# Kernel optimization log

Hardware: AMD Instinct MI355X
Metric: run time of the kernel (lower is better)

The kernel has to match this reference:

```python
import jax, jax.numpy as jnp
import numpy as np

N = 100_000      # nodes
E = 1_600_000    # edges (avg degree 16)
D_IN = 256
D_OUT = 128


def setup_inputs() -> dict:
    key = jax.random.key(0)
    ks = jax.random.split(key, 13)
    stdv = 1.0 / np.sqrt(D_OUT)      # matches reset_parameters
    std_att = 1.0                    # att_vec_* have fan 1 -> stdv 1
    std_av = 1.0 / np.sqrt(3.0)
    return {
        "x": jax.random.normal(ks[0], (N, D_IN), dtype=jnp.float32),
        "edge_src": jax.random.randint(ks[1], (E,), 0, N),
        "edge_dst": jax.random.randint(ks[2], (E,), 0, N),
        "w_low": jax.random.uniform(ks[3], (E,), dtype=jnp.float32) / 16.0,   # ~normalized adj
        "w_high": jax.random.normal(ks[4], (E,), dtype=jnp.float32) / 16.0,    # high-pass weights can be +/-
        "w_unnorm": jax.random.uniform(ks[5], (E,), dtype=jnp.float32),
        "W_low": jax.random.uniform(ks[6], (D_IN, D_OUT), jnp.float32, -stdv, stdv),
        "W_high": jax.random.uniform(ks[7], (D_IN, D_OUT), jnp.float32, -stdv, stdv),
        "W_mlp": jax.random.uniform(ks[8], (D_IN, D_OUT), jnp.float32, -stdv, stdv),
        "a_low": jax.random.uniform(ks[9], (D_OUT, 1), jnp.float32, -std_att, std_att),
        "a_high": jax.random.uniform(ks[10], (D_OUT, 1), jnp.float32, -std_att, std_att),
        "a_mlp": jax.random.uniform(ks[11], (D_OUT, 1), jnp.float32, -std_att, std_att),
        "att_vec": jax.random.uniform(ks[12], (3, 3), jnp.float32, -std_av, std_av),
    }


def _spmm(w, src, dst, h, n):
    # sparse [n,n] @ dense [n,d]: gather source rows, weight, scatter-add to dest
    return jax.ops.segment_sum(w[:, None] * h[src], dst, num_segments=n)


def reference(x, edge_src, edge_dst, w_low, w_high, w_unnorm,
              W_low, W_high, W_mlp, a_low, a_high, a_mlp, att_vec):
    n = x.shape[0]
    # variant=False path: relu(spmm(adj, x @ W))
    h_low = jax.nn.relu(_spmm(w_low, edge_src, edge_dst, x @ W_low, n))
    h_high = jax.nn.relu(_spmm(w_high, edge_src, edge_dst, x @ W_high, n))
    h_mlp = jax.nn.relu(x @ W_mlp)
    # attention3: sigmoid of per-branch scalar scores -> 3x3 mix -> softmax (T=3)
    scores = jnp.concatenate([h_low @ a_low, h_high @ a_high, h_mlp @ a_mlp], axis=1)  # [n,3]
    att = jax.nn.softmax((jax.nn.sigmoid(scores) @ att_vec) / 3.0, axis=1)
    return 3.0 * (att[:, 0:1] * h_low + att[:, 1:2] * h_high + att[:, 2:3] * h_mlp)
```

## Files before the change

### kernel.cpp

```cpp
#include <hip/hip_runtime.h>
#include <hip/hip_bf16.h>
#include <math.h>

#define D_IN   256
#define D_OUT  128
#define NHB    256

typedef __attribute__((ext_vector_type(8))) short short8;
typedef __attribute__((ext_vector_type(4))) float floatx4;

__device__ __forceinline__ unsigned short f2bf(float f) {
  union { float f; unsigned u; } v; v.f = f;
  unsigned r = v.u + 0x7fffu + ((v.u >> 16) & 1u);
  return (unsigned short)(r >> 16);
}

__global__ __launch_bounds__(512) void hist_prep_kernel(
    const float* __restrict__ Wl, const float* __restrict__ Wh,
    const float* __restrict__ Wm, unsigned short* __restrict__ Bpack,
    const int* __restrict__ dst, int* __restrict__ bh, int E, int NB1,
    int* __restrict__ ticket) {
  __shared__ int hist[1024];
  const int bid = blockIdx.x;
  const int t = threadIdx.x;
  if (bid == 0 && t == 0) *ticket = 0;
  if (bid < NHB) {
    for (int k = t; k < NB1; k += 512) hist[k] = 0;
    __syncthreads();
    const int chunk = (E + NHB - 1) / NHB;
    const int base = bid * chunk;
    const int lim = min(E, base + chunk);
    for (int e = base + t; e < lim; e += 512) atomicAdd(&hist[dst[e] >> 7], 1);
    __syncthreads();
    for (int k = t; k < NB1; k += 512) bh[k * NHB + bid] = hist[k];
  } else {
    int tt = (bid - NHB) * 512 + t;
    int j = tt & 7;
    int lane = (tt >> 3) & 63;
    int f = tt >> 9;
    int nt = f % 24, kt = f / 24;
    int k = kt * 32 + (lane >> 4) * 8 + j;
    int n_ = nt * 16 + (lane & 15);
    const float* W = (n_ < 128) ? Wl : (n_ < 256 ? Wh : Wm);
    Bpack[tt] = f2bf(W[k * D_OUT + (n_ & 127)]);
  }
}

__global__ __launch_bounds__(512) void scan_kernel(
    const int* __restrict__ bh, int* __restrict__ bhscan,
    int* __restrict__ bsum, int M, int nscan, int* __restrict__ ticket) {
  __shared__ int sd[512];
  __shared__ int lastFlag;
  const int sb = blockIdx.x;
  const int t = threadIdx.x;
  int base = sb * 2048 + t * 4;
  int v0 = base + 0 < M ? bh[base + 0] : 0;
  int v1 = base + 1 < M ? bh[base + 1] : 0;
  int v2 = base + 2 < M ? bh[base + 2] : 0;
  int v3 = base + 3 < M ? bh[base + 3] : 0;
  int tsum = v0 + v1 + v2 + v3;
  sd[t] = tsum;
  __syncthreads();
  for (int off = 1; off < 512; off <<= 1) {
    int add = (t >= off) ? sd[t - off] : 0;
    __syncthreads();
    sd[t] += add;
    __syncthreads();
  }
  int excl = sd[t] - tsum;
  if (base + 0 < M) bhscan[base + 0] = excl;
  if (base + 1 < M) bhscan[base + 1] = excl + v0;
  if (base + 2 < M) bhscan[base + 2] = excl + v0 + v1;
  if (base + 3 < M) bhscan[base + 3] = excl + v0 + v1 + v2;
  if (t == 511) {
    bsum[sb] = sd[511];
    __threadfence();
    int prev = atomicAdd(ticket, 1);
    lastFlag = (prev == nscan - 1);
  }
  __syncthreads();
  if (!lastFlag) return;
  __threadfence();
  int v = t < nscan ? bsum[t] : 0;
  sd[t] = v;
  __syncthreads();
  for (int off = 1; off < 512; off <<= 1) {
    int add = (t >= off) ? sd[t - off] : 0;
    __syncthreads();
    sd[t] += add;
    __syncthreads();
  }
  if (t < nscan) bsum[t] = sd[t] - v;
}

#define LDSROW 392
__global__ __launch_bounds__(512, 4) void gemm_sort_kernel(
    const float* __restrict__ x,
    const unsigned short* __restrict__ Bpack, unsigned short* __restrict__ Zg,
    unsigned short* __restrict__ Zm, int n_nodes, const int* __restrict__ src,
    const int* __restrict__ dst, const float* __restrict__ wlo,
    const float* __restrict__ whi, const int* __restrict__ bhscan,
    const int* __restrict__ bsum, uint2* __restrict__ tmp, int E, int NB1) {
  __shared__ unsigned short lds[16384];
  const int bid = blockIdx.x;

  int gemm_id;
  if (bid < 2 * NHB) {
    if ((bid & 1) == 0) {
      int rb = bid >> 1;
      int* cur = (int*)lds;
      int t = threadIdx.x;
      for (int k = t; k < NB1; k += 512) {
        int idx = k * NHB + rb;
        cur[k] = bhscan[idx] + bsum[idx >> 11];
      }
      __syncthreads();
      const int chunk = (E + NHB - 1) / NHB;
      const int base = rb * chunk;
      const int lim = min(E, base + chunk);
      for (int e = base + t; e < lim; e += 512) {
        int d = dst[e];
        int pos = atomicAdd(&cur[d >> 7], 1);
        unsigned wl = f2bf(wlo[e]), wh = f2bf(whi[e]);
        tmp[pos] = make_uint2((unsigned)src[e] | ((unsigned)(d & 127) << 20),
                              wl | (wh << 16));
      }
      return;
    }
    gemm_id = bid >> 1;
  } else {
    gemm_id = bid - 2 * NHB + NHB;
  }

  const int lane = threadIdx.x & 63;
  const int w = threadIdx.x >> 6;
  const int rowbase = gemm_id * 64;
  const int m16 = lane & 15, quad = lane >> 4;

  {
    const float4* xf = (const float4*)x;
#pragma unroll
    for (int i = 0; i < 4; i++) {
      int idx = i * 512 + threadIdx.x;
      int row = idx >> 5, c = idx & 31;
      int gr = rowbase + row;
      if (gr > n_nodes - 1) gr = n_nodes - 1;
      float4 f0 = xf[(size_t)gr * 64 + c * 2];
      float4 f1 = xf[(size_t)gr * 64 + c * 2 + 1];
      unsigned w0, w1, w2, w3;
      asm("v_cvt_pk_bf16_f32 %0, %1, %2" : "=v"(w0) : "v"(f0.x), "v"(f0.y));
      asm("v_cvt_pk_bf16_f32 %0, %1, %2" : "=v"(w1) : "v"(f0.z), "v"(f0.w));
      asm("v_cvt_pk_bf16_f32 %0, %1, %2" : "=v"(w2) : "v"(f1.x), "v"(f1.y));
      asm("v_cvt_pk_bf16_f32 %0, %1, %2" : "=v"(w3) : "v"(f1.z), "v"(f1.w));
      union { uint4 u; short8 s8; } cv;
      cv.u = make_uint4(w0, w1, w2, w3);
      int pc = (c & ~7) | ((c ^ row) & 7);
      ((short8*)lds)[row * 32 + pc] = cv.s8;
    }
  }
  __syncthreads();

  floatx4 acc[4][3];
#pragma unroll
  for (int s = 0; s < 4; s++)
#pragma unroll
    for (int c = 0; c < 3; c++) acc[s][c] = (floatx4)(0.f);

  const short8* bp = (const short8*)Bpack + lane;

#pragma unroll
  for (int kt = 0; kt < 8; kt++) {
    short8 a[4];
#pragma unroll
    for (int s = 0; s < 4; s++) {
      int r_ = s * 16 + m16;
      int c_ = kt * 4 + quad;
      int pc = (c_ & ~7) | ((c_ ^ r_) & 7);
      a[s] = ((const short8*)lds)[r_ * 32 + pc];
    }
#pragma unroll
    for (int c = 0; c < 3; c++) {
      short8 b = bp[(kt * 24 + w * 3 + c) * 64];
#pragma unroll
      for (int s = 0; s < 4; s++)
        acc[s][c] =
            __builtin_amdgcn_mfma_f32_16x16x32_bf16(a[s], b, acc[s][c], 0, 0, 0);
    }
  }

  __syncthreads();
  unsigned short* tile = lds;

#pragma unroll
  for (int half = 0; half < 2; half++) {
    if (half) __syncthreads();
#pragma unroll
    for (int s = 0; s < 2; s++)
#pragma unroll
      for (int c = 0; c < 3; c++)
#pragma unroll
        for (int r = 0; r < 4; r++)
          tile[(s * 16 + quad * 4 + r) * LDSROW + (w * 3 + c) * 16 + m16] =
              f2bf(acc[half * 2 + s][c][r]);
    __syncthreads();
#pragma unroll
    for (int it = 0; it < 3; it++) {
      int chunk = it * 512 + threadIdx.x;
      int row = chunk / 48, c8 = chunk % 48;
      int grow = rowbase + half * 32 + row;
      if (grow < n_nodes) {
        short8 v = *(const short8*)&tile[row * LDSROW + c8 * 8];
        if (c8 < 32)
          *(short8*)(Zg + (size_t)grow * 256 + c8 * 8) = v;
        else
          *(short8*)(Zm + (size_t)grow * 128 + (c8 - 32) * 8) = v;
      }
    }
  }
}

__global__ __launch_bounds__(512) void fine_kernel(
    const uint2* __restrict__ tmp, const int* __restrict__ bhscan,
    const int* __restrict__ bsum, uint2* __restrict__ meta,
    int* __restrict__ rowptr, int NB1, int n, int E) {
  __shared__ int fh[128];
  __shared__ int sd[128];
  __shared__ int cur[128];
  const int b = blockIdx.x;
  const int t = threadIdx.x;
  auto scanidx = [&](int i) { return bhscan[i] + bsum[i >> 11]; };
  const int s0 = scanidx(b * NHB);
  const int s1 = (b == NB1 - 1) ? E : scanidx((b + 1) * NHB);

  if (t < 128) fh[t] = 0;
  __syncthreads();
  for (int i = s0 + t; i < s1; i += 512)
    atomicAdd(&fh[(tmp[i].x >> 20) & 127], 1);
  __syncthreads();

  if (t < 128) sd[t] = fh[t];
  __syncthreads();
  for (int off = 1; off < 128; off <<= 1) {
    int add = (t >= off && t < 128) ? sd[t - off] : 0;
    __syncthreads();
    if (t < 128) sd[t] += add;
    __syncthreads();
  }
  if (t < 128) {
    int excl = sd[t] - fh[t];
    cur[t] = excl;
    int node = b * 128 + t;
    if (node < n) rowptr[node] = s0 + excl;
  }
  if (b == 0 && t == 0) rowptr[n] = E;
  __syncthreads();

  for (int i = s0 + t; i < s1; i += 512) {
    uint2 v = tmp[i];
    int d = (v.x >> 20) & 127;
    int pos = s0 + atomicAdd(&cur[d], 1);
    meta[pos] = make_uint2(v.x & 0xFFFFFu, v.y);
  }
}

__global__ __launch_bounds__(128) void node_kernel(
    const unsigned short* __restrict__ Zg, const unsigned short* __restrict__ Zm,
    const int* __restrict__ rowptr, const unsigned long long* __restrict__ meta,
    const float* __restrict__ a_low, const float* __restrict__ a_high,
    const float* __restrict__ a_mlp, const float* __restrict__ att_vec,
    float* __restrict__ out, int n_nodes) {
  int node = blockIdx.x * 2 + (threadIdx.x >> 6);
  if (node >= n_nodes) return;
  node = __builtin_amdgcn_readfirstlane(node);
  const int lane = threadIdx.x & 63;
  const int isHigh = lane >> 5;
  const int dbase = (lane & 31) * 4;
  const char* Zb = (const char*)Zg;

  const int start = rowptr[node];
  const int end = rowptr[node + 1];

  float acc0 = 0.f, acc1 = 0.f, acc2 = 0.f, acc3 = 0.f;
  auto wsel = [&](unsigned p) {
    return __uint_as_float(isHigh ? (p & 0xffff0000u) : (p << 16));
  };
  auto step = [&](uint2 z, float wv) {
    acc0 += wv * __uint_as_float(z.x << 16);
    acc1 += wv * __uint_as_float(z.x & 0xffff0000u);
    acc2 += wv * __uint_as_float(z.y << 16);
    acc3 += wv * __uint_as_float(z.y & 0xffff0000u);
  };

  int j = start;
  const int nfull = (end - start) & ~7;
  for (; j < start + nfull; j += 8) {
    unsigned long long m[8];
    uint2 z[8];
#pragma unroll
    for (int u = 0; u < 8; u++) m[u] = __builtin_nontemporal_load(&meta[j + u]);
#pragma unroll
    for (int u = 0; u < 8; u++)
      z[u] = *(const uint2*)(Zb + ((size_t)(unsigned)m[u]) * 512 + lane * 8);
#pragma unroll
    for (int u = 0; u < 8; u++) step(z[u], wsel((unsigned)(m[u] >> 32)));
  }
  for (; j < end; j++) {
    unsigned long long m0 = __builtin_nontemporal_load(&meta[j]);
    uint2 z0 = *(const uint2*)(Zb + ((size_t)(unsigned)m0) * 512 + lane * 8);
    step(z0, wsel((unsigned)(m0 >> 32)));
  }

  float h0 = fmaxf(acc0, 0.f), h1 = fmaxf(acc1, 0.f);
  float h2 = fmaxf(acc2, 0.f), h3 = fmaxf(acc3, 0.f);

  unsigned long long zmq = __builtin_nontemporal_load(
      (const unsigned long long*)((const char*)Zm + (size_t)node * 256 +
                                  (size_t)(lane & 31) * 8));
  unsigned zmx = (unsigned)zmq, zmy = (unsigned)(zmq >> 32);
  float q0 = fmaxf(__uint_as_float(zmx << 16), 0.f);
  float q1 = fmaxf(__uint_as_float(zmx & 0xffff0000u), 0.f);
  float q2 = fmaxf(__uint_as_float(zmy << 16), 0.f);
  float q3 = fmaxf(__uint_as_float(zmy & 0xffff0000u), 0.f);

  const float* av_b = isHigh ? a_high : a_low;
  float4 ab = *(const float4*)&av_b[dbase];
  float4 am = *(const float4*)&a_mlp[dbase];
  float v1 = h0 * ab.x + h1 * ab.y + h2 * ab.z + h3 * ab.w;
  float v2 = isHigh ? 0.f : (q0 * am.x + q1 * am.y + q2 * am.z + q3 * am.w);
#pragma unroll
  for (int off = 1; off < 32; off <<= 1) {
    v1 += __shfl_xor(v1, off);
    v2 += __shfl_xor(v2, off);
  }
  float s_lo = __shfl(v1, 0);
  float s_hi = __shfl(v1, 32);
  float s_ml = __shfl(v2, 0);

  float g0 = 1.f / (1.f + __expf(-s_lo));
  float g1 = 1.f / (1.f + __expf(-s_hi));
  float g2 = 1.f / (1.f + __expf(-s_ml));
  const float inv3 = 1.f / 3.f;
  float m0 = (g0 * att_vec[0] + g1 * att_vec[3] + g2 * att_vec[6]) * inv3;
  float m1 = (g0 * att_vec[1] + g1 * att_vec[4] + g2 * att_vec[7]) * inv3;
  float m2 = (g0 * att_vec[2] + g1 * att_vec[5] + g2 * att_vec[8]) * inv3;
  float mx = fmaxf(m0, fmaxf(m1, m2));
  float e0 = __expf(m0 - mx), e1 = __expf(m1 - mx), e2 = __expf(m2 - mx);
  float inv = 1.f / (e0 + e1 + e2);
  float c0 = 3.f * inv * e0, c1 = 3.f * inv * e1, c2 = 3.f * inv * e2;

  float hh0 = __shfl_xor(h0, 32);
  float hh1 = __shfl_xor(h1, 32);
  float hh2 = __shfl_xor(h2, 32);
  float hh3 = __shfl_xor(h3, 32);

  if (!isHigh) {
    floatx4 o;
    o.x = c0 * h0 + c1 * hh0 + c2 * q0;
    o.y = c0 * h1 + c1 * hh1 + c2 * q1;
    o.z = c0 * h2 + c1 * hh2 + c2 * q2;
    o.w = c0 * h3 + c1 * hh3 + c2 * q3;
    __builtin_nontemporal_store(o,
                                (floatx4*)&out[(size_t)node * D_OUT + dbase]);
  }
}

extern "C" void kernel_launch(void* const* d_in, const int* in_sizes, int n_in,
                              void* d_out, int out_size, void* d_ws,
                              size_t ws_size, hipStream_t stream) {
  const float* x    = (const float*)d_in[0];
  const int*   esrc = (const int*)d_in[1];
  const int*   edst = (const int*)d_in[2];
  const float* wlo  = (const float*)d_in[3];
  const float* whi  = (const float*)d_in[4];
  const float* Wl   = (const float*)d_in[6];
  const float* Wh   = (const float*)d_in[7];
  const float* Wm   = (const float*)d_in[8];
  const float* alo  = (const float*)d_in[9];
  const float* ahi  = (const float*)d_in[10];
  const float* amlp = (const float*)d_in[11];
  const float* av   = (const float*)d_in[12];
  float* out = (float*)d_out;

  const int N = in_sizes[0] / D_IN;
  const int E = in_sizes[1];
  const int NB1 = (N + 127) >> 7;
  const int M = NB1 * NHB;

  char* ws = (char*)d_ws;
  size_t off = 0;
  auto carve = [&](size_t bytes) -> void* {
    void* p = ws + off;
    off = (off + bytes + 255) & ~(size_t)255;
    return p;
  };
  unsigned short* Zg     = (unsigned short*)carve((size_t)N * 256 * 2);
  unsigned short* Zm     = (unsigned short*)carve((size_t)N * 128 * 2);
  unsigned short* Bpack  = (unsigned short*)carve(98304 * 2);
  int*   bh     = (int*)carve((size_t)M * 4);
  int*   bhscan = (int*)carve((size_t)M * 4);
  int*   bsum   = (int*)carve(512 * 4);
  int*   rowptr = (int*)carve((size_t)(N + 1) * 4);
  int*   ticket = (int*)carve(256);
  uint2* tmp    = (uint2*)carve((size_t)E * 8);
  uint2* meta   = (uint2*)carve((size_t)E * 8);

  int nscan = (M + 2047) / 2048;

  hist_prep_kernel<<<NHB + 192, 512, 0, stream>>>(Wl, Wh, Wm, Bpack, edst, bh,
                                                  E, NB1, ticket);
  scan_kernel<<<nscan, 512, 0, stream>>>(bh, bhscan, bsum, M, nscan, ticket);
  int ngemm = (N + 63) / 64;
  gemm_sort_kernel<<<ngemm + NHB, 512, 0, stream>>>(
      x, Bpack, Zg, Zm, N, esrc, edst, wlo, whi, bhscan, bsum, tmp, E, NB1);
  fine_kernel<<<NB1, 512, 0, stream>>>(tmp, bhscan, bsum, meta, rowptr, NB1, N,
                                       E);
  node_kernel<<<(N + 1) / 2, 128, 0, stream>>>(
      Zg, Zm, rowptr, (const unsigned long long*)meta, alo, ahi, amlp, av, out,
      N);
}
```

Measured before the change: 395.1 us.

## Split GEMM tiles across scatter and fine-sort kernels to overlap work

The dense GEMM tiles are spread over two launches. The first 1000 tiles run interleaved with the coarse edge scatter, and the rest run interleaved with the fine per-bucket sort, which before ran alone. The aim is to fill the device during the latency-bound sort phases with compute-heavy GEMM blocks and balance the two launches. The fine kernel now uses 32KB LDS and launch_bounds(512,4), which may reduce its occupancy, and the split point is a fixed constant.

```diff
diff --git a/kernel.cpp b/kernel.cpp
--- a/kernel.cpp
+++ b/kernel.cpp
@@ -94,44 +94,10 @@
 }
 
 #define LDSROW 392
-__global__ __launch_bounds__(512, 4) void gemm_sort_kernel(
-    const float* __restrict__ x,
+__device__ __forceinline__ void gemm_tile(
+    int gemm_id, unsigned short* lds, const float* __restrict__ x,
     const unsigned short* __restrict__ Bpack, unsigned short* __restrict__ Zg,
-    unsigned short* __restrict__ Zm, int n_nodes, const int* __restrict__ src,
-    const int* __restrict__ dst, const float* __restrict__ wlo,
-    const float* __restrict__ whi, const int* __restrict__ bhscan,
-    const int* __restrict__ bsum, uint2* __restrict__ tmp, int E, int NB1) {
-  __shared__ unsigned short lds[16384];
-  const int bid = blockIdx.x;
-
-  int gemm_id;
-  if (bid < 2 * NHB) {
-    if ((bid & 1) == 0) {
-      int rb = bid >> 1;
-      int* cur = (int*)lds;
-      int t = threadIdx.x;
-      for (int k = t; k < NB1; k += 512) {
-        int idx = k * NHB + rb;
-        cur[k] = bhscan[idx] + bsum[idx >> 11];
-      }
-      __syncthreads();
-      const int chunk = (E + NHB - 1) / NHB;
-      const int base = rb * chunk;
-      const int lim = min(E, base + chunk);
-      for (int e = base + t; e < lim; e += 512) {
-        int d = dst[e];
-        int pos = atomicAdd(&cur[d >> 7], 1);
-        unsigned wl = f2bf(wlo[e]), wh = f2bf(whi[e]);
-        tmp[pos] = make_uint2((unsigned)src[e] | ((unsigned)(d & 127) << 20),
-                              wl | (wh << 16));
-      }
-      return;
-    }
-    gemm_id = bid >> 1;
-  } else {
-    gemm_id = bid - 2 * NHB + NHB;
-  }
-
+    unsigned short* __restrict__ Zm, int n_nodes) {
   const int lane = threadIdx.x & 63;
   const int w = threadIdx.x >> 6;
   const int rowbase = gemm_id * 64;
@@ -219,14 +185,81 @@
   }
 }
 
-__global__ __launch_bounds__(512) void fine_kernel(
+__global__ __launch_bounds__(512, 4) void scatter_gemm_kernel(
+    const int* __restrict__ src, const int* __restrict__ dst,
+    const float* __restrict__ wlo, const float* __restrict__ whi,
+    const int* __restrict__ bhscan, const int* __restrict__ bsum,
+    uint2* __restrict__ tmp, int E, int NB1, int ngA,
+    const float* __restrict__ x, const unsigned short* __restrict__ Bpack,
+    unsigned short* __restrict__ Zg, unsigned short* __restrict__ Zm,
+    int n_nodes) {
+  __shared__ unsigned short lds[16384];
+  const int bid = blockIdx.x;
+  const int mn = min(NHB, ngA), m2 = 2 * mn;
+  int role, idx;
+  if (bid < m2) {
+    role = bid & 1;
+    idx = bid >> 1;
+  } else if (NHB < ngA) {
+    role = 1;
+    idx = bid - m2 + mn;
+  } else {
+    role = 0;
+    idx = bid - m2 + mn;
+  }
+  if (role == 0) {
+    int rb = idx;
+    int* cur = (int*)lds;
+    int t = threadIdx.x;
+    for (int k = t; k < NB1; k += 512) {
+      int i2 = k * NHB + rb;
+      cur[k] = bhscan[i2] + bsum[i2 >> 11];
+    }
+    __syncthreads();
+    const int chunk = (E + NHB - 1) / NHB;
+    const int base = rb * chunk;
+    const int lim = min(E, base + chunk);
+    for (int e = base + t; e < lim; e += 512) {
+      int d = dst[e];
+      int pos = atomicAdd(&cur[d >> 7], 1);
+      unsigned wl = f2bf(wlo[e]), wh = f2bf(whi[e]);
+      tmp[pos] = make_uint2((unsigned)src[e] | ((unsigned)(d & 127) << 20),
+                            wl | (wh << 16));
+    }
+  } else {
+    gemm_tile(idx, lds, x, Bpack, Zg, Zm, n_nodes);
+  }
+}
+
+__global__ __launch_bounds__(512, 4) void fine_gemm_kernel(
     const uint2* __restrict__ tmp, const int* __restrict__ bhscan,
     const int* __restrict__ bsum, uint2* __restrict__ meta,
-    int* __restrict__ rowptr, int NB1, int n, int E) {
-  __shared__ int fh[128];
-  __shared__ int sd[128];
-  __shared__ int cur[128];
-  const int b = blockIdx.x;
+    int* __restrict__ rowptr, int NB1, int n, int E, int ngB, int gbase,
+    const float* __restrict__ x, const unsigned short* __restrict__ Bpack,
+    unsigned short* __restrict__ Zg, unsigned short* __restrict__ Zm,
+    int n_nodes) {
+  __shared__ unsigned short lds[16384];
+  const int bid = blockIdx.x;
+  const int mn = min(NB1, ngB), m2 = 2 * mn;
+  int role, idx;
+  if (bid < m2) {
+    role = bid & 1;
+    idx = bid >> 1;
+  } else if (NB1 < ngB) {
+    role = 1;
+    idx = bid - m2 + mn;
+  } else {
+    role = 0;
+    idx = bid - m2 + mn;
+  }
+  if (role == 1) {
+    gemm_tile(gbase + idx, lds, x, Bpack, Zg, Zm, n_nodes);
+    return;
+  }
+  const int b = idx;
+  int* fh = (int*)lds;
+  int* sd = fh + 128;
+  int* cur = fh + 256;
   const int t = threadIdx.x;
   auto scanidx = [&](int i) { return bhscan[i] + bsum[i >> 11]; };
   const int s0 = scanidx(b * NHB);
@@ -405,15 +438,19 @@
   uint2* meta   = (uint2*)carve((size_t)E * 8);
 
   int nscan = (M + 2047) / 2048;
+  int ngemm = (N + 63) / 64;
+  int NGA = 1000;
+  int NGB = ngemm - NGA;
 
   hist_prep_kernel<<<NHB + 192, 512, 0, stream>>>(Wl, Wh, Wm, Bpack, edst, bh,
                                                   E, NB1, ticket);
   scan_kernel<<<nscan, 512, 0, stream>>>(bh, bhscan, bsum, M, nscan, ticket);
-  int ngemm = (N + 63) / 64;
-  gemm_sort_kernel<<<ngemm + NHB, 512, 0, stream>>>(
-      x, Bpack, Zg, Zm, N, esrc, edst, wlo, whi, bhscan, bsum, tmp, E, NB1);
-  fine_kernel<<<NB1, 512, 0, stream>>>(tmp, bhscan, bsum, meta, rowptr, NB1, N,
-                                       E);
+  scatter_gemm_kernel<<<NHB + NGA, 512, 0, stream>>>(
+      esrc, edst, wlo, whi, bhscan, bsum, tmp, E, NB1, NGA, x, Bpack, Zg, Zm,
+      N);
+  fine_gemm_kernel<<<NB1 + NGB, 512, 0, stream>>>(
+      tmp, bhscan, bsum, meta, rowptr, NB1, N, E, NGB, NGA, x, Bpack, Zg, Zm,
+      N);
   node_kernel<<<(N + 1) / 2, 128, 0, stream>>>(
       Zg, Zm, rowptr, (const unsigned long long*)meta, alo, ahi, amlp, av, out,
       N);
```

New measurement: 408.4 us. +3.4%, slower.
